# Performance work log

Measured on AMD Instinct MI355X. Metric: run time of the kernel, lower is better.

## Reference

```python
import jax, jax.numpy as jnp
import numpy as np

B, LP, LR = 16, 128, 1024
D = 128
DG = 640  # 5 * 128 concat
K = 7     # number of FC trans heads
EDGE_P = 0.05


def _gcn_block(x, adj, mask, W1, b1, W2, b2):
    # x: [B,L,DG], adj: [B,L,L] (nonzero => edge weight 1, like dense_to_sparse + GCNConv)
    A = (adj != 0).astype(x.dtype)
    L = A.shape[-1]
    eye = jnp.eye(L, dtype=x.dtype)
    Ah = jnp.maximum(A, eye)                     # add_remaining_self_loops
    deg = Ah.sum(axis=1)                         # col degree [B,L] (gcn_norm uses target index)
    dinv = jax.lax.rsqrt(deg)                    # deg >= 1 thanks to self loops
    N = Ah * dinv[:, :, None] * dinv[:, None, :] # normalized adjacency per edge (r,c)
    agg = lambda h: jnp.einsum('brc,brd->bcd', N, h)  # aggregate sources r into target c
    h1 = jax.nn.relu(agg(x @ W1) + b1)
    h2 = agg(h1 @ W2) + b2
    return jax.nn.relu(x + h2) * mask[..., None]


def _fc_trans(feature, Wt, bt):
    # feature: [B,L,DG]; Wt: [K,D,DG]; bt: [K,D]
    h = jnp.einsum('bld,kod->kblo', feature, Wt) + bt[:, None, None, :]
    h = jax.nn.relu(h)                 # FCNet [640->128], ReLU (dropout off in eval)
    return jnp.swapaxes(h, 2, 3)       # [K,B,D,L] (transpose(1,2))


def _forward(x_pep, x_ss_pep, x_2_pep, x_dense_pep, x_pretrain_pep,
             x_pro, x_ss_pro, x_2_pro, x_dense_pro, x_pretrain_pro,
             x_edge_pep, x_edge_pro, x_seqmask_pep, x_seqmask_pro,
             E_seq, E_ss, E_two, W_dpep, b_dpep, W_dpro, b_dpro,
             W_ppep, b_ppep, W_ppro, b_ppro,
             Wg_pep1, bg_pep1, Wg_pep2, bg_pep2,
             Wg_pro1, bg_pro1, Wg_pro2, bg_pro2,
             Wt_pep, bt_pep, Wt_pro, bt_pro):
    enc_pep = jnp.concatenate([
        E_seq[x_pep], E_ss[x_ss_pep], E_two[x_2_pep],
        x_dense_pep @ W_dpep + b_dpep,
        x_pretrain_pep @ W_ppep + b_ppep], axis=-1) * x_seqmask_pep[..., None]
    enc_pro = jnp.concatenate([
        E_seq[x_pro], E_ss[x_ss_pro], E_two[x_2_pro],
        x_dense_pro @ W_dpro + b_dpro,
        x_pretrain_pro @ W_ppro + b_ppro], axis=-1) * x_seqmask_pro[..., None]

    f_pep = _gcn_block(enc_pep, x_edge_pep, x_seqmask_pep, Wg_pep1, bg_pep1, Wg_pep2, bg_pep2)
    f_pro = _gcn_block(enc_pro, x_edge_pro, x_seqmask_pro, Wg_pro1, bg_pro1, Wg_pro2, bg_pro2)

    pep_vecs = _fc_trans(f_pep, Wt_pep, bt_pep)[..., None]        # [K,B,D,LP,1] (unsqueeze 3)
    pro_vecs = _fc_trans(f_pro, Wt_pro, bt_pro)[:, :, :, None, :]  # [K,B,D,1,LR] (unsqueeze 2)
    return pep_vecs, pro_vecs


def setup_inputs() -> dict:
    key = jax.random.key(0)
    ks = jax.random.split(key, 40)
    f32 = jnp.float32
    s = 0.05
    inp = {
        'x_pep': jax.random.randint(ks[0], (B, LP), 0, 25),
        'x_ss_pep': jax.random.randint(ks[1], (B, LP), 0, 73),
        'x_2_pep': jax.random.randint(ks[2], (B, LP), 0, 8),
        'x_dense_pep': jax.random.normal(ks[3], (B, LP, 3), f32),
        'x_pretrain_pep': jax.random.normal(ks[4], (B, LP, 1024), f32),
        'x_pro': jax.random.randint(ks[5], (B, LR), 0, 25),
        'x_ss_pro': jax.random.randint(ks[6], (B, LR), 0, 73),
        'x_2_pro': jax.random.randint(ks[7], (B, LR), 0, 8),
        'x_dense_pro': jax.random.normal(ks[8], (B, LR, 23), f32),
        'x_pretrain_pro': jax.random.normal(ks[9], (B, LR, 1024), f32),
        'x_edge_pep': (jax.random.uniform(ks[10], (B, LP, LP)) < EDGE_P).astype(f32),
        'x_edge_pro': (jax.random.uniform(ks[11], (B, LR, LR)) < EDGE_P).astype(f32),
        'x_seqmask_pep': jnp.ones((B, LP), f32),
        'x_seqmask_pro': jnp.ones((B, LR), f32),
        'E_seq': jax.random.normal(ks[12], (25, D), f32) * s,
        'E_ss': jax.random.normal(ks[13], (73, D), f32) * s,
        'E_two': jax.random.normal(ks[14], (8, D), f32) * s,
        'W_dpep': jax.random.normal(ks[15], (3, D), f32) * s,
        'b_dpep': jnp.zeros((D,), f32),
        'W_dpro': jax.random.normal(ks[16], (23, D), f32) * s,
        'b_dpro': jnp.zeros((D,), f32),
        'W_ppep': jax.random.normal(ks[17], (1024, D), f32) * s,
        'b_ppep': jnp.zeros((D,), f32),
        'W_ppro': jax.random.normal(ks[18], (1024, D), f32) * s,
        'b_ppro': jnp.zeros((D,), f32),
        'Wg_pep1': jax.random.normal(ks[19], (DG, DG), f32) * s,
        'bg_pep1': jnp.zeros((DG,), f32),
        'Wg_pep2': jax.random.normal(ks[20], (DG, DG), f32) * s,
        'bg_pep2': jnp.zeros((DG,), f32),
        'Wg_pro1': jax.random.normal(ks[21], (DG, DG), f32) * s,
        'bg_pro1': jnp.zeros((DG,), f32),
        'Wg_pro2': jax.random.normal(ks[22], (DG, DG), f32) * s,
        'bg_pro2': jnp.zeros((DG,), f32),
        'Wt_pep': jax.random.normal(ks[23], (K, D, DG), f32) * s,
        'bt_pep': jnp.zeros((K, D), f32),
        'Wt_pro': jax.random.normal(ks[24], (K, D, DG), f32) * s,
        'bt_pro': jnp.zeros((K, D), f32),
    }
    return inp


def reference(x_pep, x_ss_pep, x_2_pep, x_dense_pep, x_pretrain_pep,
              x_pro, x_ss_pro, x_2_pro, x_dense_pro, x_pretrain_pro,
              x_edge_pep, x_edge_pro, x_seqmask_pep, x_seqmask_pro,
              E_seq, E_ss, E_two, W_dpep, b_dpep, W_dpro, b_dpro,
              W_ppep, b_ppep, W_ppro, b_ppro,
              Wg_pep1, bg_pep1, Wg_pep2, bg_pep2,
              Wg_pro1, bg_pro1, Wg_pro2, bg_pro2,
              Wt_pep, bt_pep, Wt_pro, bt_pro):
    return _forward(x_pep, x_ss_pep, x_2_pep, x_dense_pep, x_pretrain_pep,
                    x_pro, x_ss_pro, x_2_pro, x_dense_pro, x_pretrain_pro,
                    x_edge_pep, x_edge_pro, x_seqmask_pep, x_seqmask_pro,
                    E_seq, E_ss, E_two, W_dpep, b_dpep, W_dpro, b_dpro,
                    W_ppep, b_ppep, W_ppro, b_ppro,
                    Wg_pep1, bg_pep1, Wg_pep2, bg_pep2,
                    Wg_pro1, bg_pro1, Wg_pro2, bg_pro2,
                    Wt_pep, bt_pep, Wt_pro, bt_pro)
```

## Files before the change

kernel.cpp:

```cpp
#include <hip/hip_runtime.h>
#include <hip/hip_bf16.h>

#define BSZ 16
#define LP 128
#define LR 1024
#define DD 128
#define DG 640
#define KH 7
#define SPLITK 4

typedef __bf16 bf16x8 __attribute__((ext_vector_type(8)));
typedef __bf16 bf16x4v __attribute__((ext_vector_type(4)));
typedef float f32x4 __attribute__((ext_vector_type(4)));
typedef unsigned int uint32;

template <int AF32>
__device__ __forceinline__ void mfma_core(
    const void* __restrict__ A_, int lda,
    const ushort* __restrict__ Bb, int ldb,
    int m0, int n0, int kStart, int kEnd, f32x4 (&acc)[4][4]) {
  __shared__ __align__(16) ushort As[128 * 72];
  __shared__ __align__(16) ushort Bs[128 * 72];
  int t = threadIdx.x;
  int wave = t >> 6, lane = t & 63;
  int quad = lane >> 4, l16 = lane & 15;
  int wm = (wave >> 1) * 64, wn = (wave & 1) * 64;
  int r1 = t >> 2, o1 = (t & 3) * 16;

  int4 b00, b01, b10, b11;
  int4 a00, a01, a10, a11;
  float4 af32[8];

  auto load_k = [&](int k0) {
    b00 = *(const int4*)(Bb + (size_t)(n0 + r1) * ldb + k0 + o1);
    b01 = *(const int4*)(Bb + (size_t)(n0 + r1) * ldb + k0 + o1 + 8);
    b10 = *(const int4*)(Bb + (size_t)(n0 + r1 + 64) * ldb + k0 + o1);
    b11 = *(const int4*)(Bb + (size_t)(n0 + r1 + 64) * ldb + k0 + o1 + 8);
    if (AF32) {
      const float* Af = (const float*)A_;
      #pragma unroll
      for (int s = 0; s < 8; ++s) {
        int idx = t + s * 256;
        int row = idx >> 4, c4 = (idx & 15) * 4;
        af32[s] = *(const float4*)(Af + (size_t)(m0 + row) * lda + k0 + c4);
      }
    } else {
      const ushort* Ab = (const ushort*)A_;
      a00 = *(const int4*)(Ab + (size_t)(m0 + r1) * lda + k0 + o1);
      a01 = *(const int4*)(Ab + (size_t)(m0 + r1) * lda + k0 + o1 + 8);
      a10 = *(const int4*)(Ab + (size_t)(m0 + r1 + 64) * lda + k0 + o1);
      a11 = *(const int4*)(Ab + (size_t)(m0 + r1 + 64) * lda + k0 + o1 + 8);
    }
  };

  load_k(kStart);
  for (int k0 = kStart; k0 < kEnd; k0 += 64) {
    __syncthreads();
    if (AF32) {
      #pragma unroll
      for (int s = 0; s < 8; ++s) {
        int idx = t + s * 256;
        int row = idx >> 4, c4 = (idx & 15) * 4;
        ushort4 u; __bf16 h;
        h = (__bf16)af32[s].x; u.x = *(ushort*)&h;
        h = (__bf16)af32[s].y; u.y = *(ushort*)&h;
        h = (__bf16)af32[s].z; u.z = *(ushort*)&h;
        h = (__bf16)af32[s].w; u.w = *(ushort*)&h;
        *(ushort4*)&As[row * 72 + c4] = u;
      }
    } else {
      *(int4*)&As[r1 * 72 + o1] = a00;
      *(int4*)&As[r1 * 72 + o1 + 8] = a01;
      *(int4*)&As[(r1 + 64) * 72 + o1] = a10;
      *(int4*)&As[(r1 + 64) * 72 + o1 + 8] = a11;
    }
    *(int4*)&Bs[r1 * 72 + o1] = b00;
    *(int4*)&Bs[r1 * 72 + o1 + 8] = b01;
    *(int4*)&Bs[(r1 + 64) * 72 + o1] = b10;
    *(int4*)&Bs[(r1 + 64) * 72 + o1 + 8] = b11;
    __syncthreads();
    if (k0 + 64 < kEnd) load_k(k0 + 64);
    #pragma unroll
    for (int kc = 0; kc < 2; ++kc) {
      bf16x8 af[4], bfr[4];
      #pragma unroll
      for (int fi = 0; fi < 4; ++fi)
        af[fi] = *(const bf16x8*)&As[(wm + fi * 16 + l16) * 72 + kc * 32 + quad * 8];
      #pragma unroll
      for (int fj = 0; fj < 4; ++fj)
        bfr[fj] = *(const bf16x8*)&Bs[(wn + fj * 16 + l16) * 72 + kc * 32 + quad * 8];
      #pragma unroll
      for (int fi = 0; fi < 4; ++fi)
        #pragma unroll
        for (int fj = 0; fj < 4; ++fj)
          acc[fi][fj] = __builtin_amdgcn_mfma_f32_16x16x32_bf16(
              af[fi], bfr[fj], acc[fi][fj], 0, 0, 0);
    }
  }
}

__device__ __forceinline__ void agg_core(
    const uint32* __restrict__ pb, int L,
    const ushort* __restrict__ Bb, int ldb,
    int m0, int n0, f32x4 (&acc)[4][4]) {
  __shared__ __align__(16) ushort Bs[128 * 72];
  __shared__ uint32 Aw[2][128];
  int t = threadIdx.x;
  int wave = t >> 6, lane = t & 63;
  int quad = lane >> 4, l16 = lane & 15;
  int wm = (wave >> 1) * 64, wn = (wave & 1) * 64;
  int r1 = t >> 2, o1 = (t & 3) * 16;
  int half = t >> 7, cc = t & 127;

  int4 b00, b01, b10, b11;
  uint32 w;
  auto load_k = [&](int k0) {
    b00 = *(const int4*)(Bb + (size_t)(n0 + r1) * ldb + k0 + o1);
    b01 = *(const int4*)(Bb + (size_t)(n0 + r1) * ldb + k0 + o1 + 8);
    b10 = *(const int4*)(Bb + (size_t)(n0 + r1 + 64) * ldb + k0 + o1);
    b11 = *(const int4*)(Bb + (size_t)(n0 + r1 + 64) * ldb + k0 + o1 + 8);
    w = pb[(size_t)((k0 >> 5) + half) * L + m0 + cc];
  };

  load_k(0);
  for (int k0 = 0; k0 < L; k0 += 64) {
    __syncthreads();
    *(int4*)&Bs[r1 * 72 + o1] = b00;
    *(int4*)&Bs[r1 * 72 + o1 + 8] = b01;
    *(int4*)&Bs[(r1 + 64) * 72 + o1] = b10;
    *(int4*)&Bs[(r1 + 64) * 72 + o1 + 8] = b11;
    Aw[half][cc] = w;
    __syncthreads();
    if (k0 + 64 < L) load_k(k0 + 64);
    #pragma unroll
    for (int kc = 0; kc < 2; ++kc) {
      bf16x8 af[4], bfr[4];
      #pragma unroll
      for (int fj = 0; fj < 4; ++fj)
        bfr[fj] = *(const bf16x8*)&Bs[(wn + fj * 16 + l16) * 72 + kc * 32 + quad * 8];
      #pragma unroll
      for (int fi = 0; fi < 4; ++fi) {
        uint32 bits = (Aw[kc][wm + fi * 16 + l16] >> (quad * 8)) & 0xffu;
        int4 p;
        p.x = (int)((((bits >> 0) & 1) ? 0x3F80u : 0u) | (((bits >> 1) & 1) ? 0x3F800000u : 0u));
        p.y = (int)((((bits >> 2) & 1) ? 0x3F80u : 0u) | (((bits >> 3) & 1) ? 0x3F800000u : 0u));
        p.z = (int)((((bits >> 4) & 1) ? 0x3F80u : 0u) | (((bits >> 5) & 1) ? 0x3F800000u : 0u));
        p.w = (int)((((bits >> 6) & 1) ? 0x3F80u : 0u) | (((bits >> 7) & 1) ? 0x3F800000u : 0u));
        af[fi] = *(bf16x8*)&p;
      }
      #pragma unroll
      for (int fi = 0; fi < 4; ++fi)
        #pragma unroll
        for (int fj = 0; fj < 4; ++fj)
          acc[fi][fj] = __builtin_amdgcn_mfma_f32_16x16x32_bf16(
              af[fi], bfr[fj], acc[fi][fj], 0, 0, 0);
    }
  }
}

__device__ __forceinline__ void tr_tile(const float* __restrict__ src,
                                        __bf16* __restrict__ dst,
                                        int R, int C, int cb, int rb, int t) {
  __shared__ float T[32][33];
  int r0 = rb * 32, c0 = cb * 32;
  #pragma unroll
  for (int s = 0; s < 4; ++s) {
    int idx = t + s * 256;
    int r = idx >> 5, c = idx & 31;
    T[r][c] = src[(size_t)(r0 + r) * C + c0 + c];
  }
  __syncthreads();
  #pragma unroll
  for (int s = 0; s < 4; ++s) {
    int idx = t + s * 256;
    int c = idx >> 5, r = idx & 31;
    dst[(size_t)(c0 + c) * R + r0 + r] = (__bf16)T[r][c];
  }
}

__global__ __launch_bounds__(256) void prep_weights(
    const float* __restrict__ Wppep, const float* __restrict__ Wppro,
    const float* __restrict__ Wg1p, const float* __restrict__ Wg2p,
    const float* __restrict__ Wg1r, const float* __restrict__ Wg2r,
    const float* __restrict__ Wtp, const float* __restrict__ Wtr,
    __bf16* __restrict__ WppTp, __bf16* __restrict__ WppTr,
    __bf16* __restrict__ Wg1Tp, __bf16* __restrict__ Wg2Tp,
    __bf16* __restrict__ Wg1Tr, __bf16* __restrict__ Wg2Tr,
    __bf16* __restrict__ WtBp, __bf16* __restrict__ WtBr) {
  int z = blockIdx.z, bx = blockIdx.x, t = threadIdx.x;
  if (z < 2) {
    if (bx >= 128) return;
    tr_tile(z ? Wppro : Wppep, z ? WppTr : WppTp, 1024, 128, bx % 4, bx / 4, t);
  } else if (z < 6) {
    if (bx >= 400) return;
    const float* src = (z == 2) ? Wg1p : (z == 3) ? Wg2p : (z == 4) ? Wg1r : Wg2r;
    __bf16* dst = (z == 2) ? Wg1Tp : (z == 3) ? Wg2Tp : (z == 4) ? Wg1Tr : Wg2Tr;
    tr_tile(src, dst, 640, 640, bx % 20, bx / 20, t);
  } else {
    if (bx >= 560) return;
    const float* src = (z == 6) ? Wtp : Wtr;
    __bf16* dst = (z == 6) ? WtBp : WtBr;
    int i = bx * 256 + t;
    float4 v = ((const float4*)src)[i];
    bf16x4v o;
    o.x = (__bf16)v.x; o.y = (__bf16)v.y; o.z = (__bf16)v.z; o.w = (__bf16)v.w;
    ((bf16x4v*)dst)[i] = o;
  }
}

__global__ __launch_bounds__(256) void zero_f32(float* __restrict__ p, int n) {
  int i = blockIdx.x * 256 + threadIdx.x;
  if (i < n) p[i] = 0.f;
}

__global__ __launch_bounds__(256) void rsqrt_k(const float* __restrict__ deg,
                                               float* __restrict__ dinv, int n) {
  int i = blockIdx.x * 256 + threadIdx.x;
  if (i < n) dinv[i] = rsqrtf(deg[i]);
}

__global__ __launch_bounds__(256) void prep_pack_merged(
    const float* __restrict__ adjP, const float* __restrict__ adjR,
    uint32* __restrict__ packedP, uint32* __restrict__ packedR,
    float* __restrict__ degP, float* __restrict__ degR) {
  int t = threadIdx.x;
  const float* adj; uint32* packed; float* deg;
  int b, rw, c, L;
  if (blockIdx.z < 16) {
    L = LR; b = blockIdx.z; rw = blockIdx.y; c = blockIdx.x * 256 + t;
    adj = adjR; packed = packedR; deg = degR;
  } else {
    L = LP; b = blockIdx.y; rw = blockIdx.x; c = t;
    if (b >= 16 || c >= LP) return;
    adj = adjP; packed = packedP; deg = degP;
  }
  const float* adjB = adj + (size_t)b * L * L;
  uint32 w = 0;
  int rbase = rw * 32;
  #pragma unroll 8
  for (int j = 0; j < 32; ++j) {
    float a = adjB[(size_t)(rbase + j) * L + c];
    if (a != 0.f || (rbase + j) == c) w |= (1u << j);
  }
  packed[((size_t)b * (L >> 5) + rw) * L + c] = w;
  atomicAdd(deg + b * L + c, (float)__popc(w));
}

__global__ __launch_bounds__(256) void pre_gemm(
    const float* __restrict__ XpP, const float* __restrict__ XpR,
    const __bf16* __restrict__ WppTp, const __bf16* __restrict__ WppTr,
    float* __restrict__ partP, float* __restrict__ partR) {
  int bx = blockIdx.x, s = blockIdx.y;
  int pep = bx < (BSZ * LP / 128);
  int m0 = (pep ? bx : bx - BSZ * LP / 128) * 128;
  const float* A = pep ? XpP : XpR;
  const ushort* B = (const ushort*)(pep ? WppTp : WppTr);
  int BL = pep ? BSZ * LP : BSZ * LR;
  float* part = (pep ? partP : partR) + (size_t)s * BL * DD;

  f32x4 acc[4][4];
  #pragma unroll
  for (int i = 0; i < 4; ++i)
    #pragma unroll
    for (int j = 0; j < 4; ++j) acc[i][j] = (f32x4){0.f, 0.f, 0.f, 0.f};
  mfma_core<1>(A, 1024, B, 1024, m0, 0, s * (1024 / SPLITK),
               (s + 1) * (1024 / SPLITK), acc);

  int t = threadIdx.x;
  int wave = t >> 6, lane = t & 63;
  int quad = lane >> 4, l16 = lane & 15;
  int wm = (wave >> 1) * 64, wn = (wave & 1) * 64;
  #pragma unroll
  for (int fi = 0; fi < 4; ++fi)
    #pragma unroll
    for (int r = 0; r < 4; ++r) {
      int m = m0 + wm + fi * 16 + quad * 4 + r;
      #pragma unroll
      for (int fj = 0; fj < 4; ++fj) {
        int n = wn + fj * 16 + l16;
        part[(size_t)m * DD + n] = acc[fi][fj][r];
      }
    }
}

__global__ __launch_bounds__(128) void encoder_merged(
    const int* __restrict__ xsP, const int* __restrict__ xssP,
    const int* __restrict__ x2P, const float* __restrict__ xdP,
    const float* __restrict__ WdP, const float* __restrict__ bdP,
    const float* __restrict__ maskP, const float* __restrict__ partP,
    const float* __restrict__ bppP, __bf16* __restrict__ encP,
    const int* __restrict__ xsR, const int* __restrict__ xssR,
    const int* __restrict__ x2R, const float* __restrict__ xdR,
    const float* __restrict__ WdR, const float* __restrict__ bdR,
    const float* __restrict__ maskR, const float* __restrict__ partR,
    const float* __restrict__ bppR, __bf16* __restrict__ encR,
    const float* __restrict__ Eseq, const float* __restrict__ Ess,
    const float* __restrict__ Etwo) {
  int gw = blockIdx.x;
  int t = threadIdx.x;
  int pep = gw < BSZ * LP;
  int row = pep ? gw : gw - BSZ * LP;
  int BL = pep ? BSZ * LP : BSZ * LR;
  int Kd = pep ? 3 : 23;
  const int* xs = pep ? xsP : xsR;
  const int* xss = pep ? xssP : xssR;
  const int* x2 = pep ? x2P : x2R;
  const float* xd = pep ? xdP : xdR;
  const float* Wd = pep ? WdP : WdR;
  const float* bd = pep ? bdP : bdR;
  const float* mask = pep ? maskP : maskR;
  const float* part = pep ? partP : partR;
  const float* bpp = pep ? bppP : bppR;
  __bf16* enc = pep ? encP : encR;

  float m = mask[row];
  int i0 = xs[row], i1 = xss[row], i2 = x2[row];
  __bf16* e = enc + (size_t)row * DG;
  e[t]        = (__bf16)(Eseq[i0 * DD + t] * m);
  e[DD + t]   = (__bf16)(Ess[i1 * DD + t] * m);
  e[2*DD + t] = (__bf16)(Etwo[i2 * DD + t] * m);
  float acc = bd[t];
  const float* xr = xd + (size_t)row * Kd;
  for (int i = 0; i < Kd; ++i) acc = fmaf(xr[i], Wd[i * DD + t], acc);
  e[3*DD + t] = (__bf16)(acc * m);
  float p = bpp[t];
  #pragma unroll
  for (int s = 0; s < SPLITK; ++s)
    p += part[(size_t)s * BL * DD + (size_t)row * DD + t];
  e[4*DD + t] = (__bf16)(p * m);
}

__global__ __launch_bounds__(256) void linT_merged(
    const __bf16* __restrict__ WgTp, const __bf16* __restrict__ srcP,
    const float* __restrict__ dinvP, __bf16* __restrict__ dstP,
    const __bf16* __restrict__ WgTr, const __bf16* __restrict__ srcR,
    const float* __restrict__ dinvR, __bf16* __restrict__ dstR) {
  int bx = blockIdx.x;
  int pep = bx < (BSZ * LP / 128);
  int n0 = (pep ? bx : bx - BSZ * LP / 128) * 128;
  int m0 = blockIdx.y * 128;
  int BL = pep ? BSZ * LP : BSZ * LR;
  const __bf16* A = pep ? WgTp : WgTr;
  const ushort* B = (const ushort*)(pep ? srcP : srcR);
  const float* dinv = pep ? dinvP : dinvR;
  __bf16* dst = pep ? dstP : dstR;

  f32x4 acc[4][4];
  #pragma unroll
  for (int i = 0; i < 4; ++i)
    #pragma unroll
    for (int j = 0; j < 4; ++j) acc[i][j] = (f32x4){0.f, 0.f, 0.f, 0.f};
  mfma_core<0>(A, DG, B, DG, m0, n0, 0, DG, acc);

  int t = threadIdx.x;
  int wave = t >> 6, lane = t & 63;
  int quad = lane >> 4, l16 = lane & 15;
  int wm = (wave >> 1) * 64, wn = (wave & 1) * 64;
  #pragma unroll
  for (int fi = 0; fi < 4; ++fi)
    #pragma unroll
    for (int r = 0; r < 4; ++r) {
      int m = m0 + wm + fi * 16 + quad * 4 + r;
      #pragma unroll
      for (int fj = 0; fj < 4; ++fj) {
        int n = n0 + wn + fj * 16 + l16;
        dst[(size_t)m * BL + n] = (__bf16)(acc[fi][fj][r] * dinv[n]);
      }
    }
}

__global__ __launch_bounds__(256) void agg_merged(
    const uint32* __restrict__ packedP, const __bf16* __restrict__ XtP,
    const float* __restrict__ dinvP, const float* __restrict__ biasP,
    const __bf16* __restrict__ encEP, const float* __restrict__ maskP,
    __bf16* __restrict__ YP,
    const uint32* __restrict__ packedR, const __bf16* __restrict__ XtR,
    const float* __restrict__ dinvR, const float* __restrict__ biasR,
    const __bf16* __restrict__ encER, const float* __restrict__ maskR,
    __bf16* __restrict__ YR) {
  int bx = blockIdx.x;
  int b = bx / 5;
  int n0 = (bx % 5) * 128;
  int pep = (blockIdx.y == 0);
  int L = pep ? LP : LR;
  int BL = BSZ * L;
  int m0 = pep ? 0 : (blockIdx.y - 1) * 128;
  const uint32* pb = (pep ? packedP : packedR) + (size_t)b * (L >> 5) * L;
  const ushort* Bb = (const ushort*)(pep ? XtP : XtR) + (size_t)b * L;
  const float* dinv = pep ? dinvP : dinvR;
  const float* bias = pep ? biasP : biasR;
  const __bf16* encE = pep ? encEP : encER;
  const float* mask = pep ? maskP : maskR;
  __bf16* Y = pep ? YP : YR;

  f32x4 acc[4][4];
  #pragma unroll
  for (int i = 0; i < 4; ++i)
    #pragma unroll
    for (int j = 0; j < 4; ++j) acc[i][j] = (f32x4){0.f, 0.f, 0.f, 0.f};
  agg_core(pb, L, Bb, BL, m0, n0, acc);

  int t = threadIdx.x;
  int wave = t >> 6, lane = t & 63;
  int quad = lane >> 4, l16 = lane & 15;
  int wm = (wave >> 1) * 64, wn = (wave & 1) * 64;
  int gRow = b * L;
  #pragma unroll
  for (int fi = 0; fi < 4; ++fi)
    #pragma unroll
    for (int r = 0; r < 4; ++r) {
      int m = m0 + wm + fi * 16 + quad * 4 + r;
      int gi = gRow + m;
      float di = dinv[gi];
      float rm = mask ? mask[gi] : 1.f;
      #pragma unroll
      for (int fj = 0; fj < 4; ++fj) {
        int n = n0 + wn + fj * 16 + l16;
        float v = acc[fi][fj][r] * di + bias[n];
        if (encE) v += (float)encE[(size_t)gi * DG + n];
        v = fmaxf(v, 0.f);
        v *= rm;
        Y[(size_t)gi * DG + n] = (__bf16)v;
      }
    }
}

__global__ __launch_bounds__(256) void fct_merged(
    const __bf16* __restrict__ WtBp, const float* __restrict__ btp,
    const __bf16* __restrict__ Yp, float* __restrict__ outP,
    const __bf16* __restrict__ WtBr, const float* __restrict__ btr,
    const __bf16* __restrict__ Yr, float* __restrict__ outR) {
  int kh = blockIdx.y;
  int pro = (blockIdx.z < 16);
  const __bf16* A;
  const ushort* B;
  const float* bt;
  int n0;
  if (pro) {
    A = WtBr + (size_t)kh * DD * DG;
    B = (const ushort*)(Yr + (size_t)blockIdx.z * LR * DG);
    bt = btr;
    n0 = blockIdx.x * 128;
  } else {
    A = WtBp + (size_t)kh * DD * DG;
    B = (const ushort*)Yp;
    bt = btp;
    n0 = ((blockIdx.z - 16) * 8 + blockIdx.x) * 128;
  }

  f32x4 acc[4][4];
  #pragma unroll
  for (int i = 0; i < 4; ++i)
    #pragma unroll
    for (int j = 0; j < 4; ++j) acc[i][j] = (f32x4){0.f, 0.f, 0.f, 0.f};
  mfma_core<0>(A, DG, B, DG, 0, n0, 0, DG, acc);

  int t = threadIdx.x;
  int wave = t >> 6, lane = t & 63;
  int quad = lane >> 4, l16 = lane & 15;
  int wm = (wave >> 1) * 64, wn = (wave & 1) * 64;
  #pragma unroll
  for (int fi = 0; fi < 4; ++fi)
    #pragma unroll
    for (int r = 0; r < 4; ++r) {
      int m = wm + fi * 16 + quad * 4 + r;
      float bb = bt[kh * DD + m];
      #pragma unroll
      for (int fj = 0; fj < 4; ++fj) {
        int n = n0 + wn + fj * 16 + l16;
        float v = fmaxf(acc[fi][fj][r] + bb, 0.f);
        if (pro) {
          outR[((size_t)(kh * BSZ + blockIdx.z) * DD + m) * LR + n] = v;
        } else {
          int b = n >> 7, l = n & 127;
          outP[((size_t)(kh * BSZ + b) * DD + m) * LP + l] = v;
        }
      }
    }
}

extern "C" void kernel_launch(void* const* d_in, const int* in_sizes, int n_in,
                              void* d_out, int out_size, void* d_ws, size_t ws_size,
                              hipStream_t stream) {
  const int*   x_pep          = (const int*)d_in[0];
  const int*   x_ss_pep       = (const int*)d_in[1];
  const int*   x_2_pep        = (const int*)d_in[2];
  const float* x_dense_pep    = (const float*)d_in[3];
  const float* x_pretrain_pep = (const float*)d_in[4];
  const int*   x_pro          = (const int*)d_in[5];
  const int*   x_ss_pro       = (const int*)d_in[6];
  const int*   x_2_pro        = (const int*)d_in[7];
  const float* x_dense_pro    = (const float*)d_in[8];
  const float* x_pretrain_pro = (const float*)d_in[9];
  const float* x_edge_pep     = (const float*)d_in[10];
  const float* x_edge_pro     = (const float*)d_in[11];
  const float* mask_pep       = (const float*)d_in[12];
  const float* mask_pro       = (const float*)d_in[13];
  const float* E_seq          = (const float*)d_in[14];
  const float* E_ss           = (const float*)d_in[15];
  const float* E_two          = (const float*)d_in[16];
  const float* W_dpep         = (const float*)d_in[17];
  const float* b_dpep         = (const float*)d_in[18];
  const float* W_dpro         = (const float*)d_in[19];
  const float* b_dpro         = (const float*)d_in[20];
  const float* W_ppep         = (const float*)d_in[21];
  const float* b_ppep         = (const float*)d_in[22];
  const float* W_ppro         = (const float*)d_in[23];
  const float* b_ppro         = (const float*)d_in[24];
  const float* Wg_pep1        = (const float*)d_in[25];
  const float* bg_pep1        = (const float*)d_in[26];
  const float* Wg_pep2        = (const float*)d_in[27];
  const float* bg_pep2        = (const float*)d_in[28];
  const float* Wg_pro1        = (const float*)d_in[29];
  const float* bg_pro1        = (const float*)d_in[30];
  const float* Wg_pro2        = (const float*)d_in[31];
  const float* bg_pro2        = (const float*)d_in[32];
  const float* Wt_pep         = (const float*)d_in[33];
  const float* bt_pep         = (const float*)d_in[34];
  const float* Wt_pro         = (const float*)d_in[35];
  const float* bt_pro         = (const float*)d_in[36];

  float* out = (float*)d_out;
  const int BLp = BSZ * LP;
  const int BLr = BSZ * LR;
  const size_t out_pro_off = (size_t)KH * BSZ * DD * LP;

  char* w = (char*)d_ws;
  __bf16* encBp  = (__bf16*)w; w += (size_t)BLp * DG * 2;
  __bf16* encBr  = (__bf16*)w; w += (size_t)BLr * DG * 2;
  __bf16* bufATp = (__bf16*)w; w += (size_t)DG * BLp * 2;
  __bf16* bufATr = (__bf16*)w; w += (size_t)DG * BLr * 2;
  __bf16* bufYp  = (__bf16*)w; w += (size_t)BLp * DG * 2;
  __bf16* bufYr  = (__bf16*)w; w += (size_t)BLr * DG * 2;
  __bf16* WppTp  = (__bf16*)w; w += (size_t)DD * 1024 * 2;
  __bf16* WppTr  = (__bf16*)w; w += (size_t)DD * 1024 * 2;
  __bf16* Wg1Tp  = (__bf16*)w; w += (size_t)DG * DG * 2;
  __bf16* Wg2Tp  = (__bf16*)w; w += (size_t)DG * DG * 2;
  __bf16* Wg1Tr  = (__bf16*)w; w += (size_t)DG * DG * 2;
  __bf16* Wg2Tr  = (__bf16*)w; w += (size_t)DG * DG * 2;
  __bf16* WtBp   = (__bf16*)w; w += (size_t)KH * DD * DG * 2;
  __bf16* WtBr   = (__bf16*)w; w += (size_t)KH * DD * DG * 2;
  uint32* packedP = (uint32*)w; w += (size_t)BSZ * (LP / 32) * LP * 4;
  uint32* packedR = (uint32*)w; w += (size_t)BSZ * (LR / 32) * LR * 4;
  float* degP  = (float*)w; w += (size_t)BLp * 4;
  float* degR  = (float*)w; w += (size_t)BLr * 4;
  float* dinvP = (float*)w; w += (size_t)BLp * 4;
  float* dinvR = (float*)w; w += (size_t)BLr * 4;
  float* partP = (float*)w; w += (size_t)SPLITK * BLp * DD * 4;
  float* partR = (float*)w; w += (size_t)SPLITK * BLr * DD * 4;

  prep_weights<<<dim3(560, 1, 8), 256, 0, stream>>>(
      W_ppep, W_ppro, Wg_pep1, Wg_pep2, Wg_pro1, Wg_pro2, Wt_pep, Wt_pro,
      WppTp, WppTr, Wg1Tp, Wg2Tp, Wg1Tr, Wg2Tr, WtBp, WtBr);
  zero_f32<<<(BLp + BLr) / 256, 256, 0, stream>>>(degP, BLp + BLr);
  prep_pack_merged<<<dim3(4, 32, 17), 256, 0, stream>>>(
      x_edge_pep, x_edge_pro, packedP, packedR, degP, degR);
  rsqrt_k<<<(BLp + BLr) / 256, 256, 0, stream>>>(degP, dinvP, BLp + BLr);
  pre_gemm<<<dim3((BLp + BLr) / 128, SPLITK), 256, 0, stream>>>(
      x_pretrain_pep, x_pretrain_pro, WppTp, WppTr, partP, partR);
  encoder_merged<<<BLp + BLr, 128, 0, stream>>>(
      x_pep, x_ss_pep, x_2_pep, x_dense_pep, W_dpep, b_dpep, mask_pep, partP,
      b_ppep, encBp,
      x_pro, x_ss_pro, x_2_pro, x_dense_pro, W_dpro, b_dpro, mask_pro, partR,
      b_ppro, encBr,
      E_seq, E_ss, E_two);
  linT_merged<<<dim3((BLp + BLr) / 128, DG / 128), 256, 0, stream>>>(
      Wg1Tp, encBp, dinvP, bufATp, Wg1Tr, encBr, dinvR, bufATr);
  agg_merged<<<dim3(80, 9), 256, 0, stream>>>(
      packedP, bufATp, dinvP, bg_pep1, nullptr, nullptr, bufYp,
      packedR, bufATr, dinvR, bg_pro1, nullptr, nullptr, bufYr);
  linT_merged<<<dim3((BLp + BLr) / 128, DG / 128), 256, 0, stream>>>(
      Wg2Tp, bufYp, dinvP, bufATp, Wg2Tr, bufYr, dinvR, bufATr);
  agg_merged<<<dim3(80, 9), 256, 0, stream>>>(
      packedP, bufATp, dinvP, bg_pep2, encBp, mask_pep, bufYp,
      packedR, bufATr, dinvR, bg_pro2, encBr, mask_pro, bufYr);
  fct_merged<<<dim3(LR / 128, KH, 18), 256, 0, stream>>>(
      WtBp, bt_pep, bufYp, out,
      WtBr, bt_pro, bufYr, out + out_pro_off);
}
```

Before: 470.3 us.

## Use direct global-to-LDS loads for bf16 GEMM and aggregation tiles

Replaces the register-staged global→LDS copies in the bf16 GEMM core and the adjacency aggregation core with global_load_lds 16-byte direct loads into unpadded 64-wide LDS tiles. This removes the VGPR round trip and the LDS store instructions. The cost is the register prefetch of the next k-tile, so loads are no longer overlapped with compute, and an extra barrier is added per iteration. Dropping the padding may also cause LDS bank conflicts on fragment reads. The f32-input path used by pre_gemm keeps the old register-staged scheme.

Measured after the change: 495.8 us. 5.4% more time.

```diff
diff --git a/kernel.cpp b/kernel.cpp
--- a/kernel.cpp
+++ b/kernel.cpp
@@ -14,9 +14,57 @@
 typedef float f32x4 __attribute__((ext_vector_type(4)));
 typedef unsigned int uint32;
 
-template <int AF32>
-__device__ __forceinline__ void mfma_core(
-    const void* __restrict__ A_, int lda,
+__device__ __forceinline__ void gl16(const void* g, void* l) {
+  __builtin_amdgcn_global_load_lds(
+      (const __attribute__((address_space(1))) unsigned int*)g,
+      (__attribute__((address_space(3))) unsigned int*)l, 16, 0, 0);
+}
+
+__device__ __forceinline__ void mfma_core_lds(
+    const ushort* __restrict__ Ab, int lda,
+    const ushort* __restrict__ Bb, int ldb,
+    int m0, int n0, int kStart, int kEnd, f32x4 (&acc)[4][4]) {
+  __shared__ __align__(16) ushort As[128 * 64];
+  __shared__ __align__(16) ushort Bs[128 * 64];
+  int t = threadIdx.x;
+  int wave = t >> 6, lane = t & 63;
+  int quad = lane >> 4, l16 = lane & 15;
+  int wm = (wave >> 1) * 64, wn = (wave & 1) * 64;
+
+  int row0 = (wave * 256 + lane) >> 3;
+  int s0 = lane & 7;
+  const ushort* aBase = Ab + (size_t)(m0 + row0) * lda + s0 * 8;
+  const ushort* bBase = Bb + (size_t)(n0 + row0) * ldb + s0 * 8;
+
+  for (int k0 = kStart; k0 < kEnd; k0 += 64) {
+    #pragma unroll
+    for (int i = 0; i < 4; ++i) {
+      gl16(aBase + (size_t)i * 8 * lda + k0, &As[wave * 2048 + i * 512]);
+      gl16(bBase + (size_t)i * 8 * ldb + k0, &Bs[wave * 2048 + i * 512]);
+    }
+    __syncthreads();
+    #pragma unroll
+    for (int kc = 0; kc < 2; ++kc) {
+      bf16x8 af[4], bfr[4];
+      #pragma unroll
+      for (int fi = 0; fi < 4; ++fi)
+        af[fi] = *(const bf16x8*)&As[(wm + fi * 16 + l16) * 64 + kc * 32 + quad * 8];
+      #pragma unroll
+      for (int fj = 0; fj < 4; ++fj)
+        bfr[fj] = *(const bf16x8*)&Bs[(wn + fj * 16 + l16) * 64 + kc * 32 + quad * 8];
+      #pragma unroll
+      for (int fi = 0; fi < 4; ++fi)
+        #pragma unroll
+        for (int fj = 0; fj < 4; ++fj)
+          acc[fi][fj] = __builtin_amdgcn_mfma_f32_16x16x32_bf16(
+              af[fi], bfr[fj], acc[fi][fj], 0, 0, 0);
+    }
+    __syncthreads();
+  }
+}
+
+__device__ __forceinline__ void mfma_core_f32(
+    const float* __restrict__ Af, int lda,
     const ushort* __restrict__ Bb, int ldb,
     int m0, int n0, int kStart, int kEnd, f32x4 (&acc)[4][4]) {
   __shared__ __align__(16) ushort As[128 * 72];
@@ -28,7 +76,6 @@
   int r1 = t >> 2, o1 = (t & 3) * 16;
 
   int4 b00, b01, b10, b11;
-  int4 a00, a01, a10, a11;
   float4 af32[8];
 
   auto load_k = [&](int k0) {
@@ -36,43 +83,27 @@
     b01 = *(const int4*)(Bb + (size_t)(n0 + r1) * ldb + k0 + o1 + 8);
     b10 = *(const int4*)(Bb + (size_t)(n0 + r1 + 64) * ldb + k0 + o1);
     b11 = *(const int4*)(Bb + (size_t)(n0 + r1 + 64) * ldb + k0 + o1 + 8);
-    if (AF32) {
-      const float* Af = (const float*)A_;
-      #pragma unroll
-      for (int s = 0; s < 8; ++s) {
-        int idx = t + s * 256;
-        int row = idx >> 4, c4 = (idx & 15) * 4;
-        af32[s] = *(const float4*)(Af + (size_t)(m0 + row) * lda + k0 + c4);
-      }
-    } else {
-      const ushort* Ab = (const ushort*)A_;
-      a00 = *(const int4*)(Ab + (size_t)(m0 + r1) * lda + k0 + o1);
-      a01 = *(const int4*)(Ab + (size_t)(m0 + r1) * lda + k0 + o1 + 8);
-      a10 = *(const int4*)(Ab + (size_t)(m0 + r1 + 64) * lda + k0 + o1);
-      a11 = *(const int4*)(Ab + (size_t)(m0 + r1 + 64) * lda + k0 + o1 + 8);
+    #pragma unroll
+    for (int s = 0; s < 8; ++s) {
+      int idx = t + s * 256;
+      int row = idx >> 4, c4 = (idx & 15) * 4;
+      af32[s] = *(const float4*)(Af + (size_t)(m0 + row) * lda + k0 + c4);
     }
   };
 
   load_k(kStart);
   for (int k0 = kStart; k0 < kEnd; k0 += 64) {
     __syncthreads();
-    if (AF32) {
-      #pragma unroll
-      for (int s = 0; s < 8; ++s) {
-        int idx = t + s * 256;
-        int row = idx >> 4, c4 = (idx & 15) * 4;
-        ushort4 u; __bf16 h;
-        h = (__bf16)af32[s].x; u.x = *(ushort*)&h;
-        h = (__bf16)af32[s].y; u.y = *(ushort*)&h;
-        h = (__bf16)af32[s].z; u.z = *(ushort*)&h;
-        h = (__bf16)af32[s].w; u.w = *(ushort*)&h;
-        *(ushort4*)&As[row * 72 + c4] = u;
-      }
-    } else {
-      *(int4*)&As[r1 * 72 + o1] = a00;
-      *(int4*)&As[r1 * 72 + o1 + 8] = a01;
-      *(int4*)&As[(r1 + 64) * 72 + o1] = a10;
-      *(int4*)&As[(r1 + 64) * 72 + o1 + 8] = a11;
+    #pragma unroll
+    for (int s = 0; s < 8; ++s) {
+      int idx = t + s * 256;
+      int row = idx >> 4, c4 = (idx & 15) * 4;
+      ushort4 u; __bf16 h;
+      h = (__bf16)af32[s].x; u.x = *(ushort*)&h;
+      h = (__bf16)af32[s].y; u.y = *(ushort*)&h;
+      h = (__bf16)af32[s].z; u.z = *(ushort*)&h;
+      h = (__bf16)af32[s].w; u.w = *(ushort*)&h;
+      *(ushort4*)&As[row * 72 + c4] = u;
     }
     *(int4*)&Bs[r1 * 72 + o1] = b00;
     *(int4*)&Bs[r1 * 72 + o1 + 8] = b01;
@@ -103,41 +134,31 @@
     const uint32* __restrict__ pb, int L,
     const ushort* __restrict__ Bb, int ldb,
     int m0, int n0, f32x4 (&acc)[4][4]) {
-  __shared__ __align__(16) ushort Bs[128 * 72];
+  __shared__ __align__(16) ushort Bs[128 * 64];
   __shared__ uint32 Aw[2][128];
   int t = threadIdx.x;
   int wave = t >> 6, lane = t & 63;
   int quad = lane >> 4, l16 = lane & 15;
   int wm = (wave >> 1) * 64, wn = (wave & 1) * 64;
-  int r1 = t >> 2, o1 = (t & 3) * 16;
   int half = t >> 7, cc = t & 127;
 
-  int4 b00, b01, b10, b11;
-  uint32 w;
-  auto load_k = [&](int k0) {
-    b00 = *(const int4*)(Bb + (size_t)(n0 + r1) * ldb + k0 + o1);
-    b01 = *(const int4*)(Bb + (size_t)(n0 + r1) * ldb + k0 + o1 + 8);
-    b10 = *(const int4*)(Bb + (size_t)(n0 + r1 + 64) * ldb + k0 + o1);
-    b11 = *(const int4*)(Bb + (size_t)(n0 + r1 + 64) * ldb + k0 + o1 + 8);
-    w = pb[(size_t)((k0 >> 5) + half) * L + m0 + cc];
-  };
-
-  load_k(0);
+  int row0 = (wave * 256 + lane) >> 3;
+  int s0 = lane & 7;
+  const ushort* bBase = Bb + (size_t)(n0 + row0) * ldb + s0 * 8;
+  const uint32* pbBase = pb + (size_t)half * L + m0 + cc;
+
   for (int k0 = 0; k0 < L; k0 += 64) {
+    #pragma unroll
+    for (int i = 0; i < 4; ++i)
+      gl16(bBase + (size_t)i * 8 * ldb + k0, &Bs[wave * 2048 + i * 512]);
+    Aw[half][cc] = pbBase[(size_t)(k0 >> 5) * L];
     __syncthreads();
-    *(int4*)&Bs[r1 * 72 + o1] = b00;
-    *(int4*)&Bs[r1 * 72 + o1 + 8] = b01;
-    *(int4*)&Bs[(r1 + 64) * 72 + o1] = b10;
-    *(int4*)&Bs[(r1 + 64) * 72 + o1 + 8] = b11;
-    Aw[half][cc] = w;
-    __syncthreads();
-    if (k0 + 64 < L) load_k(k0 + 64);
     #pragma unroll
     for (int kc = 0; kc < 2; ++kc) {
       bf16x8 af[4], bfr[4];
       #pragma unroll
       for (int fj = 0; fj < 4; ++fj)
-        bfr[fj] = *(const bf16x8*)&Bs[(wn + fj * 16 + l16) * 72 + kc * 32 + quad * 8];
+        bfr[fj] = *(const bf16x8*)&Bs[(wn + fj * 16 + l16) * 64 + kc * 32 + quad * 8];
       #pragma unroll
       for (int fi = 0; fi < 4; ++fi) {
         uint32 bits = (Aw[kc][wm + fi * 16 + l16] >> (quad * 8)) & 0xffu;
@@ -155,6 +176,7 @@
           acc[fi][fj] = __builtin_amdgcn_mfma_f32_16x16x32_bf16(
               af[fi], bfr[fj], acc[fi][fj], 0, 0, 0);
     }
+    __syncthreads();
   }
 }
 
@@ -263,8 +285,8 @@
   for (int i = 0; i < 4; ++i)
     #pragma unroll
     for (int j = 0; j < 4; ++j) acc[i][j] = (f32x4){0.f, 0.f, 0.f, 0.f};
-  mfma_core<1>(A, 1024, B, 1024, m0, 0, s * (1024 / SPLITK),
-               (s + 1) * (1024 / SPLITK), acc);
+  mfma_core_f32(A, 1024, B, 1024, m0, 0, s * (1024 / SPLITK),
+                (s + 1) * (1024 / SPLITK), acc);
 
   int t = threadIdx.x;
   int wave = t >> 6, lane = t & 63;
@@ -340,7 +362,7 @@
   int n0 = (pep ? bx : bx - BSZ * LP / 128) * 128;
   int m0 = blockIdx.y * 128;
   int BL = pep ? BSZ * LP : BSZ * LR;
-  const __bf16* A = pep ? WgTp : WgTr;
+  const ushort* A = (const ushort*)(pep ? WgTp : WgTr);
   const ushort* B = (const ushort*)(pep ? srcP : srcR);
   const float* dinv = pep ? dinvP : dinvR;
   __bf16* dst = pep ? dstP : dstR;
@@ -350,7 +372,7 @@
   for (int i = 0; i < 4; ++i)
     #pragma unroll
     for (int j = 0; j < 4; ++j) acc[i][j] = (f32x4){0.f, 0.f, 0.f, 0.f};
-  mfma_core<0>(A, DG, B, DG, m0, n0, 0, DG, acc);
+  mfma_core_lds(A, DG, B, DG, m0, n0, 0, DG, acc);
 
   int t = threadIdx.x;
   int wave = t >> 6, lane = t & 63;
@@ -432,17 +454,17 @@
     const __bf16* __restrict__ Yr, float* __restrict__ outR) {
   int kh = blockIdx.y;
   int pro = (blockIdx.z < 16);
-  const __bf16* A;
+  const ushort* A;
   const ushort* B;
   const float* bt;
   int n0;
   if (pro) {
-    A = WtBr + (size_t)kh * DD * DG;
+    A = (const ushort*)(WtBr + (size_t)kh * DD * DG);
     B = (const ushort*)(Yr + (size_t)blockIdx.z * LR * DG);
     bt = btr;
     n0 = blockIdx.x * 128;
   } else {
-    A = WtBp + (size_t)kh * DD * DG;
+    A = (const ushort*)(WtBp + (size_t)kh * DD * DG);
     B = (const ushort*)Yp;
     bt = btp;
     n0 = ((blockIdx.z - 16) * 8 + blockIdx.x) * 128;
@@ -453,7 +475,7 @@
   for (int i = 0; i < 4; ++i)
     #pragma unroll
     for (int j = 0; j < 4; ++j) acc[i][j] = (f32x4){0.f, 0.f, 0.f, 0.f};
-  mfma_core<0>(A, DG, B, DG, 0, n0, 0, DG, acc);
+  mfma_core_lds(A, DG, B, DG, 0, n0, 0, DG, acc);
 
   int t = threadIdx.x;
   int wave = t >> 6, lane = t & 63;
```
